# Optimization experiments

Hardware: AMD Instinct MI355X
Metric: run time of the kernel (lower is better)

Reference implementation:

```python
import jax, jax.numpy as jnp
import numpy as np

B, S, D, H = 2, 2048, 1024, 16
DK = D // H


def setup_inputs() -> dict:
    key = jax.random.key(0)
    ks = jax.random.split(key, 11)
    s = 1.0 / np.sqrt(D)
    inp = {
        "q": jax.random.normal(ks[0], (B, S, D), jnp.float32),
        "k": jax.random.normal(ks[1], (B, S, D), jnp.float32),
        "v": jax.random.normal(ks[2], (B, S, D), jnp.float32),
        "mask": jnp.tril(jnp.ones((S, S), jnp.int32))[None, None],  # causal [1,1,S,S]
        "w_q": jax.random.normal(ks[3], (D, D), jnp.float32) * s,
        "b_q": jax.random.normal(ks[4], (D,), jnp.float32) * 0.01,
        "w_k": jax.random.normal(ks[5], (D, D), jnp.float32) * s,
        "b_k": jax.random.normal(ks[6], (D,), jnp.float32) * 0.01,
        "w_v": jax.random.normal(ks[7], (D, D), jnp.float32) * s,
        "b_v": jax.random.normal(ks[8], (D,), jnp.float32) * 0.01,
        "w_o": jax.random.normal(ks[9], (D, D), jnp.float32) * s,
        "b_o": jax.random.normal(ks[10], (D,), jnp.float32) * 0.01,
    }
    return inp


def reference(q, k, v, mask, w_q, b_q, w_k, b_k, w_v, b_v, w_o, b_o):
    # Linear projections (torch Linear: x @ W.T + b)
    query = q @ w_q.T + b_q  # [B,S,D]
    key_ = k @ w_k.T + b_k
    value = v @ w_v.T + b_v
    # split heads -> [B,H,S,DK]
    def split(x):
        return x.reshape(B, S, H, DK).transpose(0, 2, 1, 3)
    qh, kh, vh = split(query), split(key_), split(value)
    scores = jnp.einsum("bhqd,bhkd->bhqk", qh, kh) / jnp.sqrt(jnp.float32(DK))
    scores = jnp.where(mask == 0, jnp.float32(-1e9), scores)
    attn = jax.nn.softmax(scores, axis=-1)
    out = jnp.einsum("bhqk,bhkd->bhqd", attn, vh)  # [B,H,S,DK]
    out = out.transpose(0, 2, 1, 3).reshape(B, S, D)
    return out @ w_o.T + b_o
```

## Files before the change

kernel.cpp:

```cpp
#include <hip/hip_runtime.h>


typedef __attribute__((ext_vector_type(8))) short bf16x8;
typedef __attribute__((ext_vector_type(4))) float floatx4;
typedef __attribute__((ext_vector_type(4))) unsigned short u16x4;

#define S_LEN 2048
#define D_MODEL 1024
#define N_HEADS 16
#define D_HEAD 64
#define M_ROWS 4096
#define QSCALE 0.18033688011112042f

__device__ __forceinline__ unsigned short f32_to_bf16(float f) {
  unsigned int u = __builtin_bit_cast(unsigned int, f);
  u += 0x7FFFu + ((u >> 16) & 1u);
  return (unsigned short)(u >> 16);
}

__device__ __forceinline__ void async_lds16(const unsigned short* g, unsigned short* l) {
  __builtin_amdgcn_global_load_lds(
      (const __attribute__((address_space(1))) unsigned int*)g,
      (__attribute__((address_space(3))) unsigned int*)l, 16, 0, 0);
}

__global__ __launch_bounds__(256) void cvt_w(
    const float* __restrict__ w0, const float* __restrict__ w1,
    const float* __restrict__ w2, const float* __restrict__ w3,
    unsigned short* __restrict__ dst) {
  const int z = blockIdx.y;
  const float* src = (z == 0) ? w0 : (z == 1) ? w1 : (z == 2) ? w2 : w3;
  unsigned short* d = dst + ((long)z << 20);
  const int n4 = 1 << 18;
  for (int i = blockIdx.x * 256 + threadIdx.x; i < n4; i += gridDim.x * 256) {
    float4 f = ((const float4*)src)[i];
    u16x4 o;
    o[0] = f32_to_bf16(f.x); o[1] = f32_to_bf16(f.y);
    o[2] = f32_to_bf16(f.z); o[3] = f32_to_bf16(f.w);
    ((u16x4*)d)[i] = o;
  }
}

__global__ __launch_bounds__(256) void cvt_x(
    const float* __restrict__ x0, const float* __restrict__ x1,
    const float* __restrict__ x2, unsigned short* __restrict__ dst) {
  const int z = blockIdx.y;
  const float* src = (z == 0) ? x0 : (z == 1) ? x1 : x2;
  unsigned short* d = dst + (long)z * M_ROWS * D_MODEL;
  const int n4 = (M_ROWS * D_MODEL) / 4;
  for (int i = blockIdx.x * 256 + threadIdx.x; i < n4; i += gridDim.x * 256) {
    float4 f = ((const float4*)src)[i];
    u16x4 o;
    o[0] = f32_to_bf16(f.x); o[1] = f32_to_bf16(f.y);
    o[2] = f32_to_bf16(f.z); o[3] = f32_to_bf16(f.w);
    ((u16x4*)d)[i] = o;
  }
}

#define GK 1024
#define GN 1024

template <bool XPRE>
__global__ __launch_bounds__(256, 3) void qkv_gemm(
    const float* __restrict__ Xq, const float* __restrict__ Xk, const float* __restrict__ Xv,
    const unsigned short* __restrict__ Xb,
    const unsigned short* __restrict__ Wb,
    const float* __restrict__ bq, const float* __restrict__ bk, const float* __restrict__ bv,
    unsigned short* __restrict__ Yq, unsigned short* __restrict__ Yk,
    unsigned short* __restrict__ Yvt) {
  __shared__ __align__(16) unsigned short As[128 * 64];
  __shared__ __align__(16) unsigned short Bs[128 * 64];

  const int z = blockIdx.z;
  const unsigned short* W = Wb + ((long)z << 20);
  const float* bias = (z == 0) ? bq : ((z == 1) ? bk : bv);

  const int r0 = blockIdx.x * 128;
  const int n0 = blockIdx.y * 128;
  const int tid = threadIdx.x;
  const int lane = tid & 63;
  const int wave = tid >> 6;
  const int quad = lane >> 4;
  const int ln = lane & 15;
  const int wm = (wave >> 1) * 64;
  const int wn = (wave & 1) * 64;

  floatx4 acc[4][4];
#pragma unroll
  for (int i = 0; i < 4; i++)
#pragma unroll
    for (int j = 0; j < 4; j++) acc[i][j] = (floatx4){0.f, 0.f, 0.f, 0.f};

  const int srow = (lane >> 3);
  const int scol8 = (lane & 7) * 8;
  const unsigned short* ApH = nullptr;
  const float* ApF = nullptr;
  if constexpr (XPRE) {
    ApH = Xb + (long)z * M_ROWS * D_MODEL;
  } else {
    ApF = (z == 0) ? Xq : ((z == 1) ? Xk : Xv);
  }

  for (int k0 = 0; k0 < GK; k0 += 64) {
    __syncthreads();
    if constexpr (XPRE) {
#pragma unroll
      for (int i = 0; i < 4; i++) {
        const int row = wave * 32 + i * 8;
        async_lds16(ApH + (long)(r0 + row + srow) * GK + k0 + scol8,
                    As + row * 64);
        async_lds16(W + (long)(n0 + row + srow) * GK + k0 + scol8,
                    Bs + row * 64);
      }
    } else {
      const int arow = tid >> 1;
      const int acol = (tid & 1) * 32;
      unsigned short ua[32] __attribute__((aligned(16)));
      float fa[32] __attribute__((aligned(16)));
#pragma unroll
      for (int c = 0; c < 8; c++)
        *(float4*)(fa + c * 4) = *(const float4*)(ApF + (long)(r0 + arow) * GK + k0 + acol + c * 4);
#pragma unroll
      for (int j = 0; j < 32; j++) ua[j] = f32_to_bf16(fa[j]);
      *(float4*)(As + arow * 64 + acol) = *(float4*)(ua);
      *(float4*)(As + arow * 64 + acol + 8) = *(float4*)(ua + 8);
      *(float4*)(As + arow * 64 + acol + 16) = *(float4*)(ua + 16);
      *(float4*)(As + arow * 64 + acol + 24) = *(float4*)(ua + 24);
#pragma unroll
      for (int i = 0; i < 4; i++) {
        const int row = wave * 32 + i * 8;
        async_lds16(W + (long)(n0 + row + srow) * GK + k0 + scol8,
                    Bs + row * 64);
      }
    }
    __syncthreads();

#pragma unroll
    for (int ks = 0; ks < 64; ks += 32) {
      bf16x8 af[4], bfr[4];
#pragma unroll
      for (int mt = 0; mt < 4; mt++)
        af[mt] = *(const bf16x8*)(As + (wm + mt * 16 + ln) * 64 + ks + quad * 8);
#pragma unroll
      for (int nt = 0; nt < 4; nt++)
        bfr[nt] = *(const bf16x8*)(Bs + (wn + nt * 16 + ln) * 64 + ks + quad * 8);
#pragma unroll
      for (int mt = 0; mt < 4; mt++)
#pragma unroll
        for (int nt = 0; nt < 4; nt++)
          acc[mt][nt] = __builtin_amdgcn_mfma_f32_16x16x32_bf16(af[mt], bfr[nt], acc[mt][nt], 0, 0, 0);
    }
  }

#pragma unroll
  for (int nt = 0; nt < 4; nt++) {
    const int n = n0 + wn + nt * 16 + ln;
    const float bv = bias[n];
#pragma unroll
    for (int mt = 0; mt < 4; mt++) {
      const int r = r0 + wm + mt * 16 + quad * 4;
      if (z == 2) {
        u16x4 pk;
#pragma unroll
        for (int reg = 0; reg < 4; reg++) pk[reg] = f32_to_bf16(acc[mt][nt][reg] + bv);
        *(u16x4*)(Yvt + (long)n * M_ROWS + r) = pk;
      } else if (z == 0) {
#pragma unroll
        for (int reg = 0; reg < 4; reg++)
          Yq[(long)(r + reg) * GN + n] = f32_to_bf16((acc[mt][nt][reg] + bv) * QSCALE);
      } else {
#pragma unroll
        for (int reg = 0; reg < 4; reg++)
          Yk[(long)(r + reg) * GN + n] = f32_to_bf16(acc[mt][nt][reg] + bv);
      }
    }
  }
}

__global__ __launch_bounds__(256, 3) void out_gemm(
    const unsigned short* __restrict__ X,
    const unsigned short* __restrict__ W,
    const float* __restrict__ bias,
    float* __restrict__ Y) {
  __shared__ __align__(16) unsigned short As[64 * 64];
  __shared__ __align__(16) unsigned short Bs[128 * 64];

  const int r0 = blockIdx.x * 64;
  const int n0 = blockIdx.y * 128;
  const int tid = threadIdx.x;
  const int lane = tid & 63;
  const int wave = tid >> 6;
  const int quad = lane >> 4;
  const int ln = lane & 15;
  const int wm = (wave >> 1) * 32;
  const int wn = (wave & 1) * 64;

  floatx4 acc[2][4];
#pragma unroll
  for (int i = 0; i < 2; i++)
#pragma unroll
    for (int j = 0; j < 4; j++) acc[i][j] = (floatx4){0.f, 0.f, 0.f, 0.f};

  const int srow = (lane >> 3);
  const int scol8 = (lane & 7) * 8;

  for (int k0 = 0; k0 < GK; k0 += 64) {
    __syncthreads();
#pragma unroll
    for (int i = 0; i < 2; i++) {
      const int row = wave * 16 + i * 8;
      async_lds16(X + (long)(r0 + row + srow) * GK + k0 + scol8, As + row * 64);
    }
#pragma unroll
    for (int i = 0; i < 4; i++) {
      const int row = wave * 32 + i * 8;
      async_lds16(W + (long)(n0 + row + srow) * GK + k0 + scol8, Bs + row * 64);
    }
    __syncthreads();

#pragma unroll
    for (int ks = 0; ks < 64; ks += 32) {
      bf16x8 af[2], bfr[4];
#pragma unroll
      for (int mt = 0; mt < 2; mt++)
        af[mt] = *(const bf16x8*)(As + (wm + mt * 16 + ln) * 64 + ks + quad * 8);
#pragma unroll
      for (int nt = 0; nt < 4; nt++)
        bfr[nt] = *(const bf16x8*)(Bs + (wn + nt * 16 + ln) * 64 + ks + quad * 8);
#pragma unroll
      for (int mt = 0; mt < 2; mt++)
#pragma unroll
        for (int nt = 0; nt < 4; nt++)
          acc[mt][nt] = __builtin_amdgcn_mfma_f32_16x16x32_bf16(af[mt], bfr[nt], acc[mt][nt], 0, 0, 0);
    }
  }

#pragma unroll
  for (int nt = 0; nt < 4; nt++) {
    const int n = n0 + wn + nt * 16 + ln;
    const float bv = bias[n];
#pragma unroll
    for (int mt = 0; mt < 2; mt++) {
      const int r = r0 + wm + mt * 16 + quad * 4;
#pragma unroll
      for (int reg = 0; reg < 4; reg++)
        Y[(long)(r + reg) * GN + n] = acc[mt][nt][reg] + bv;
    }
  }
}

#define PSTR 72

__global__ __launch_bounds__(64, 2) void attn_causal(
    const unsigned short* __restrict__ Q,
    const unsigned short* __restrict__ K,
    const unsigned short* __restrict__ Vt,
    unsigned short* __restrict__ O) {
  __shared__ __align__(16) unsigned short PbA[16 * PSTR];
  __shared__ __align__(16) unsigned short PbB[16 * PSTR];

  const int bh = blockIdx.x;
  const int pr = blockIdx.y;
  const int b = bh >> 4;
  const int h = bh & 15;

  const int lane = threadIdx.x;
  const int quad = lane >> 4;
  const int ln = lane & 15;

  const int s1 = pr, s2 = 127 - pr;
  const int q0A = s1 * 16, q0B = s2 * 16;
  const int nkt1 = (s1 >> 2) + 1;
  const int nkt2 = (s2 >> 2) + 1;

  const unsigned short* Qb = Q + (long)b * S_LEN * D_MODEL + h * D_HEAD;
  const unsigned short* Kb = K + (long)b * S_LEN * D_MODEL + h * D_HEAD;
  const unsigned short* Vb = Vt + (long)h * D_HEAD * M_ROWS + b * S_LEN;

  bf16x8 qfA[2], qfB[2];
  qfA[0] = *(const bf16x8*)(Qb + (long)(q0A + ln) * D_MODEL + quad * 8);
  qfA[1] = *(const bf16x8*)(Qb + (long)(q0A + ln) * D_MODEL + 32 + quad * 8);
  qfB[0] = *(const bf16x8*)(Qb + (long)(q0B + ln) * D_MODEL + quad * 8);
  qfB[1] = *(const bf16x8*)(Qb + (long)(q0B + ln) * D_MODEL + 32 + quad * 8);

  float mA = -1e30f, lA = 0.f, mB = -1e30f, lB = 0.f;
  floatx4 oA[4], oB[4];
#pragma unroll
  for (int nt = 0; nt < 4; nt++) {
    oA[nt] = (floatx4){0.f, 0.f, 0.f, 0.f};
    oB[nt] = (floatx4){0.f, 0.f, 0.f, 0.f};
  }

  auto loadKV = [&](bf16x8 (&kf)[4][2], bf16x8 (&vf)[4][2], int kt) {
    const int kv0 = kt * 64;
#pragma unroll
    for (int ct = 0; ct < 4; ct++) {
      const unsigned short* kp = Kb + (long)(kv0 + ct * 16 + ln) * D_MODEL + quad * 8;
      kf[ct][0] = *(const bf16x8*)(kp);
      kf[ct][1] = *(const bf16x8*)(kp + 32);
      const unsigned short* vp = Vb + (long)(ct * 16 + ln) * M_ROWS + kv0 + quad * 8;
      vf[ct][0] = *(const bf16x8*)(vp);
      vf[ct][1] = *(const bf16x8*)(vp + 32);
    }
  };

  auto iter = [&](bf16x8 (&kf)[4][2], bf16x8 (&vf)[4][2], int kt) {
    const int kv0 = kt * 64;
    const bool aAct = (kt < nkt1);

    floatx4 sB[4], sA[4];
#pragma unroll
    for (int ct = 0; ct < 4; ct++) {
      sB[ct] = (floatx4){0.f, 0.f, 0.f, 0.f};
      sB[ct] = __builtin_amdgcn_mfma_f32_16x16x32_bf16(kf[ct][0], qfB[0], sB[ct], 0, 0, 0);
      sB[ct] = __builtin_amdgcn_mfma_f32_16x16x32_bf16(kf[ct][1], qfB[1], sB[ct], 0, 0, 0);
    }
    if (aAct) {
#pragma unroll
      for (int ct = 0; ct < 4; ct++) {
        sA[ct] = (floatx4){0.f, 0.f, 0.f, 0.f};
        sA[ct] = __builtin_amdgcn_mfma_f32_16x16x32_bf16(kf[ct][0], qfA[0], sA[ct], 0, 0, 0);
        sA[ct] = __builtin_amdgcn_mfma_f32_16x16x32_bf16(kf[ct][1], qfA[1], sA[ct], 0, 0, 0);
      }
    }

    {
      float tmax = -1e30f;
      if (kt == nkt2 - 1) {
        const int qg = q0B + ln;
#pragma unroll
        for (int ct = 0; ct < 4; ct++) {
          const int kvb = kv0 + ct * 16 + quad * 4;
#pragma unroll
          for (int reg = 0; reg < 4; reg++) {
            float sv = sB[ct][reg];
            if (kvb + reg > qg) sv = -1e30f;
            sB[ct][reg] = sv;
            tmax = fmaxf(tmax, sv);
          }
        }
      } else {
#pragma unroll
        for (int ct = 0; ct < 4; ct++)
#pragma unroll
          for (int reg = 0; reg < 4; reg++) tmax = fmaxf(tmax, sB[ct][reg]);
      }
      tmax = fmaxf(tmax, __shfl_xor(tmax, 16, 64));
      tmax = fmaxf(tmax, __shfl_xor(tmax, 32, 64));
      const float mnew = fmaxf(mB, tmax);
      const float alpha = exp2f(mB - mnew);
      mB = mnew;
      float rsum = 0.f;
#pragma unroll
      for (int ct = 0; ct < 4; ct++) {
        u16x4 pk;
#pragma unroll
        for (int reg = 0; reg < 4; reg++) {
          const float p = exp2f(sB[ct][reg] - mB);
          rsum += p;
          pk[reg] = f32_to_bf16(p);
        }
        *(u16x4*)(PbB + ln * PSTR + ct * 16 + quad * 4) = pk;
      }
      rsum += __shfl_xor(rsum, 16, 64);
      rsum += __shfl_xor(rsum, 32, 64);
      lB = lB * alpha + rsum;
#pragma unroll
      for (int nt = 0; nt < 4; nt++)
#pragma unroll
        for (int reg = 0; reg < 4; reg++) oB[nt][reg] *= alpha;
    }

    if (aAct) {
      float tmax = -1e30f;
      if (kt == nkt1 - 1) {
        const int qg = q0A + ln;
#pragma unroll
        for (int ct = 0; ct < 4; ct++) {
          const int kvb = kv0 + ct * 16 + quad * 4;
#pragma unroll
          for (int reg = 0; reg < 4; reg++) {
            float sv = sA[ct][reg];
            if (kvb + reg > qg) sv = -1e30f;
            sA[ct][reg] = sv;
            tmax = fmaxf(tmax, sv);
          }
        }
      } else {
#pragma unroll
        for (int ct = 0; ct < 4; ct++)
#pragma unroll
          for (int reg = 0; reg < 4; reg++) tmax = fmaxf(tmax, sA[ct][reg]);
      }
      tmax = fmaxf(tmax, __shfl_xor(tmax, 16, 64));
      tmax = fmaxf(tmax, __shfl_xor(tmax, 32, 64));
      const float mnew = fmaxf(mA, tmax);
      const float alpha = exp2f(mA - mnew);
      mA = mnew;
      float rsum = 0.f;
#pragma unroll
      for (int ct = 0; ct < 4; ct++) {
        u16x4 pk;
#pragma unroll
        for (int reg = 0; reg < 4; reg++) {
          const float p = exp2f(sA[ct][reg] - mA);
          rsum += p;
          pk[reg] = f32_to_bf16(p);
        }
        *(u16x4*)(PbA + ln * PSTR + ct * 16 + quad * 4) = pk;
      }
      rsum += __shfl_xor(rsum, 16, 64);
      rsum += __shfl_xor(rsum, 32, 64);
      lA = lA * alpha + rsum;
#pragma unroll
      for (int nt = 0; nt < 4; nt++)
#pragma unroll
        for (int reg = 0; reg < 4; reg++) oA[nt][reg] *= alpha;
    }

    __builtin_amdgcn_wave_barrier();

    {
      bf16x8 p0 = *(const bf16x8*)(PbB + ln * PSTR + quad * 8);
      bf16x8 p1 = *(const bf16x8*)(PbB + ln * PSTR + 32 + quad * 8);
#pragma unroll
      for (int nt = 0; nt < 4; nt++) {
        oB[nt] = __builtin_amdgcn_mfma_f32_16x16x32_bf16(vf[nt][0], p0, oB[nt], 0, 0, 0);
        oB[nt] = __builtin_amdgcn_mfma_f32_16x16x32_bf16(vf[nt][1], p1, oB[nt], 0, 0, 0);
      }
    }
    if (aAct) {
      bf16x8 p0 = *(const bf16x8*)(PbA + ln * PSTR + quad * 8);
      bf16x8 p1 = *(const bf16x8*)(PbA + ln * PSTR + 32 + quad * 8);
#pragma unroll
      for (int nt = 0; nt < 4; nt++) {
        oA[nt] = __builtin_amdgcn_mfma_f32_16x16x32_bf16(vf[nt][0], p0, oA[nt], 0, 0, 0);
        oA[nt] = __builtin_amdgcn_mfma_f32_16x16x32_bf16(vf[nt][1], p1, oA[nt], 0, 0, 0);
      }
    }
    __builtin_amdgcn_wave_barrier();
  };

  bf16x8 kf0[4][2], vf0[4][2], kf1[4][2], vf1[4][2];
  loadKV(kf0, vf0, 0);
#pragma unroll 1
  for (int kt = 0; kt < nkt2; kt += 2) {
    if (kt + 1 < nkt2) loadKV(kf1, vf1, kt + 1);
    iter(kf0, vf0, kt);
    if (kt + 1 >= nkt2) break;
    if (kt + 2 < nkt2) loadKV(kf0, vf0, kt + 2);
    iter(kf1, vf1, kt + 1);
  }

  {
    const float inv = 1.0f / lA;
    unsigned short* op = O + (long)b * S_LEN * D_MODEL + (long)(q0A + ln) * D_MODEL + h * D_HEAD;
#pragma unroll
    for (int nt = 0; nt < 4; nt++) {
      u16x4 pk;
#pragma unroll
      for (int reg = 0; reg < 4; reg++) pk[reg] = f32_to_bf16(oA[nt][reg] * inv);
      *(u16x4*)(op + nt * 16 + quad * 4) = pk;
    }
  }
  {
    const float inv = 1.0f / lB;
    unsigned short* op = O + (long)b * S_LEN * D_MODEL + (long)(q0B + ln) * D_MODEL + h * D_HEAD;
#pragma unroll
    for (int nt = 0; nt < 4; nt++) {
      u16x4 pk;
#pragma unroll
      for (int reg = 0; reg < 4; reg++) pk[reg] = f32_to_bf16(oB[nt][reg] * inv);
      *(u16x4*)(op + nt * 16 + quad * 4) = pk;
    }
  }
}

extern "C" void kernel_launch(void* const* d_in, const int* in_sizes, int n_in,
                              void* d_out, int out_size, void* d_ws, size_t ws_size,
                              hipStream_t stream) {
  const float* q = (const float*)d_in[0];
  const float* k = (const float*)d_in[1];
  const float* v = (const float*)d_in[2];
  const float* w_q = (const float*)d_in[4];
  const float* b_q = (const float*)d_in[5];
  const float* w_k = (const float*)d_in[6];
  const float* b_k = (const float*)d_in[7];
  const float* w_v = (const float*)d_in[8];
  const float* b_v = (const float*)d_in[9];
  const float* w_o = (const float*)d_in[10];
  const float* b_o = (const float*)d_in[11];
  float* out = (float*)d_out;

  unsigned short* ws = (unsigned short*)d_ws;
  const long NE = (long)M_ROWS * D_MODEL;
  const bool xpre = (ws_size >= (size_t)7 * NE * sizeof(unsigned short));

  unsigned short *Qp, *Kp, *Vpt, *AO, *Wb, *Xb;
  if (xpre) {
    Qp = ws;
    Kp = ws + NE;
    Vpt = ws + 2 * NE;
    Wb = ws + 3 * NE;
    Xb = ws + 4 * NE;
    AO = ws + 4 * NE;
  } else {
    Qp = ws;
    Kp = ws + NE;
    Vpt = ws + 2 * NE;
    AO = ws + 3 * NE;
    Wb = ws + 4 * NE;
    Xb = nullptr;
  }

  cvt_w<<<dim3(256, 4), 256, 0, stream>>>(w_q, w_k, w_v, w_o, Wb);
  if (xpre) {
    cvt_x<<<dim3(512, 3), 256, 0, stream>>>(q, k, v, Xb);
    qkv_gemm<true><<<dim3(M_ROWS / 128, GN / 128, 3), 256, 0, stream>>>(
        q, k, v, Xb, Wb, b_q, b_k, b_v, Qp, Kp, Vpt);
  } else {
    qkv_gemm<false><<<dim3(M_ROWS / 128, GN / 128, 3), 256, 0, stream>>>(
        q, k, v, nullptr, Wb, b_q, b_k, b_v, Qp, Kp, Vpt);
  }
  attn_causal<<<dim3(2 * N_HEADS, 64), 64, 0, stream>>>(Qp, Kp, Vpt, AO);
  out_gemm<<<dim3(M_ROWS / 64, GN / 128), 256, 0, stream>>>(AO, Wb + 3 * (1 << 20), b_o, out);
}
```

Before: 282.2 us.

## Pad row strides of intermediate bf16 buffers to avoid channel/bank conflicts

Every bf16 intermediate (converted weights, converted inputs, Q, K, attention output) now uses a row stride of 1088 elements instead of 1024, and the transposed V uses 4160 instead of 4096. The aim is to break power-of-two strides that send many rows to the same memory channels or cache sets during the strided GEMM and attention loads. The convert kernels now launch one block per row to write the padded layout. The cost is a larger workspace, slightly less contiguous data, and a different xpre size threshold, which could disable the pre-conversion path if the workspace is too small.

```diff
diff --git a/kernel.cpp b/kernel.cpp
--- a/kernel.cpp
+++ b/kernel.cpp
@@ -12,6 +12,9 @@
 #define M_ROWS 4096
 #define QSCALE 0.18033688011112042f
 
+#define XSTR 1088
+#define VSTR 4160
+
 __device__ __forceinline__ unsigned short f32_to_bf16(float f) {
   unsigned int u = __builtin_bit_cast(unsigned int, f);
   u += 0x7FFFu + ((u >> 16) & 1u);
@@ -28,33 +31,31 @@
     const float* __restrict__ w0, const float* __restrict__ w1,
     const float* __restrict__ w2, const float* __restrict__ w3,
     unsigned short* __restrict__ dst) {
+  const int row = blockIdx.x;
   const int z = blockIdx.y;
-  const float* src = (z == 0) ? w0 : (z == 1) ? w1 : (z == 2) ? w2 : w3;
-  unsigned short* d = dst + ((long)z << 20);
-  const int n4 = 1 << 18;
-  for (int i = blockIdx.x * 256 + threadIdx.x; i < n4; i += gridDim.x * 256) {
-    float4 f = ((const float4*)src)[i];
-    u16x4 o;
-    o[0] = f32_to_bf16(f.x); o[1] = f32_to_bf16(f.y);
-    o[2] = f32_to_bf16(f.z); o[3] = f32_to_bf16(f.w);
-    ((u16x4*)d)[i] = o;
-  }
+  const float* src = ((z == 0) ? w0 : (z == 1) ? w1 : (z == 2) ? w2 : w3) + (long)row * 1024;
+  unsigned short* d = dst + (long)z * 1024 * XSTR + (long)row * XSTR;
+  const int tid = threadIdx.x;
+  float4 f = ((const float4*)src)[tid];
+  u16x4 o;
+  o[0] = f32_to_bf16(f.x); o[1] = f32_to_bf16(f.y);
+  o[2] = f32_to_bf16(f.z); o[3] = f32_to_bf16(f.w);
+  *(u16x4*)(d + tid * 4) = o;
 }
 
 __global__ __launch_bounds__(256) void cvt_x(
     const float* __restrict__ x0, const float* __restrict__ x1,
     const float* __restrict__ x2, unsigned short* __restrict__ dst) {
+  const int row = blockIdx.x;
   const int z = blockIdx.y;
-  const float* src = (z == 0) ? x0 : (z == 1) ? x1 : x2;
-  unsigned short* d = dst + (long)z * M_ROWS * D_MODEL;
-  const int n4 = (M_ROWS * D_MODEL) / 4;
-  for (int i = blockIdx.x * 256 + threadIdx.x; i < n4; i += gridDim.x * 256) {
-    float4 f = ((const float4*)src)[i];
-    u16x4 o;
-    o[0] = f32_to_bf16(f.x); o[1] = f32_to_bf16(f.y);
-    o[2] = f32_to_bf16(f.z); o[3] = f32_to_bf16(f.w);
-    ((u16x4*)d)[i] = o;
-  }
+  const float* src = ((z == 0) ? x0 : (z == 1) ? x1 : x2) + (long)row * 1024;
+  unsigned short* d = dst + (long)z * M_ROWS * XSTR + (long)row * XSTR;
+  const int tid = threadIdx.x;
+  float4 f = ((const float4*)src)[tid];
+  u16x4 o;
+  o[0] = f32_to_bf16(f.x); o[1] = f32_to_bf16(f.y);
+  o[2] = f32_to_bf16(f.z); o[3] = f32_to_bf16(f.w);
+  *(u16x4*)(d + tid * 4) = o;
 }
 
 #define GK 1024
@@ -72,7 +73,7 @@
   __shared__ __align__(16) unsigned short Bs[128 * 64];
 
   const int z = blockIdx.z;
-  const unsigned short* W = Wb + ((long)z << 20);
+  const unsigned short* W = Wb + (long)z * 1024 * XSTR;
   const float* bias = (z == 0) ? bq : ((z == 1) ? bk : bv);
 
   const int r0 = blockIdx.x * 128;
@@ -96,7 +97,7 @@
   const unsigned short* ApH = nullptr;
   const float* ApF = nullptr;
   if constexpr (XPRE) {
-    ApH = Xb + (long)z * M_ROWS * D_MODEL;
+    ApH = Xb + (long)z * M_ROWS * XSTR;
   } else {
     ApF = (z == 0) ? Xq : ((z == 1) ? Xk : Xv);
   }
@@ -107,9 +108,9 @@
 #pragma unroll
       for (int i = 0; i < 4; i++) {
         const int row = wave * 32 + i * 8;
-        async_lds16(ApH + (long)(r0 + row + srow) * GK + k0 + scol8,
+        async_lds16(ApH + (long)(r0 + row + srow) * XSTR + k0 + scol8,
                     As + row * 64);
-        async_lds16(W + (long)(n0 + row + srow) * GK + k0 + scol8,
+        async_lds16(W + (long)(n0 + row + srow) * XSTR + k0 + scol8,
                     Bs + row * 64);
       }
     } else {
@@ -129,7 +130,7 @@
 #pragma unroll
       for (int i = 0; i < 4; i++) {
         const int row = wave * 32 + i * 8;
-        async_lds16(W + (long)(n0 + row + srow) * GK + k0 + scol8,
+        async_lds16(W + (long)(n0 + row + srow) * XSTR + k0 + scol8,
                     Bs + row * 64);
       }
     }
@@ -163,15 +164,15 @@
         u16x4 pk;
 #pragma unroll
         for (int reg = 0; reg < 4; reg++) pk[reg] = f32_to_bf16(acc[mt][nt][reg] + bv);
-        *(u16x4*)(Yvt + (long)n * M_ROWS + r) = pk;
+        *(u16x4*)(Yvt + (long)n * VSTR + r) = pk;
       } else if (z == 0) {
 #pragma unroll
         for (int reg = 0; reg < 4; reg++)
-          Yq[(long)(r + reg) * GN + n] = f32_to_bf16((acc[mt][nt][reg] + bv) * QSCALE);
+          Yq[(long)(r + reg) * XSTR + n] = f32_to_bf16((acc[mt][nt][reg] + bv) * QSCALE);
       } else {
 #pragma unroll
         for (int reg = 0; reg < 4; reg++)
-          Yk[(long)(r + reg) * GN + n] = f32_to_bf16(acc[mt][nt][reg] + bv);
+          Yk[(long)(r + reg) * XSTR + n] = f32_to_bf16(acc[mt][nt][reg] + bv);
       }
     }
   }
@@ -209,12 +210,12 @@
 #pragma unroll
     for (int i = 0; i < 2; i++) {
       const int row = wave * 16 + i * 8;
-      async_lds16(X + (long)(r0 + row + srow) * GK + k0 + scol8, As + row * 64);
+      async_lds16(X + (long)(r0 + row + srow) * XSTR + k0 + scol8, As + row * 64);
     }
 #pragma unroll
     for (int i = 0; i < 4; i++) {
       const int row = wave * 32 + i * 8;
-      async_lds16(W + (long)(n0 + row + srow) * GK + k0 + scol8, Bs + row * 64);
+      async_lds16(W + (long)(n0 + row + srow) * XSTR + k0 + scol8, Bs + row * 64);
     }
     __syncthreads();
 
@@ -273,15 +274,15 @@
   const int nkt1 = (s1 >> 2) + 1;
   const int nkt2 = (s2 >> 2) + 1;
 
-  const unsigned short* Qb = Q + (long)b * S_LEN * D_MODEL + h * D_HEAD;
-  const unsigned short* Kb = K + (long)b * S_LEN * D_MODEL + h * D_HEAD;
-  const unsigned short* Vb = Vt + (long)h * D_HEAD * M_ROWS + b * S_LEN;
+  const unsigned short* Qb = Q + (long)b * S_LEN * XSTR + h * D_HEAD;
+  const unsigned short* Kb = K + (long)b * S_LEN * XSTR + h * D_HEAD;
+  const unsigned short* Vb = Vt + (long)h * D_HEAD * VSTR + b * S_LEN;
 
   bf16x8 qfA[2], qfB[2];
-  qfA[0] = *(const bf16x8*)(Qb + (long)(q0A + ln) * D_MODEL + quad * 8);
-  qfA[1] = *(const bf16x8*)(Qb + (long)(q0A + ln) * D_MODEL + 32 + quad * 8);
-  qfB[0] = *(const bf16x8*)(Qb + (long)(q0B + ln) * D_MODEL + quad * 8);
-  qfB[1] = *(const bf16x8*)(Qb + (long)(q0B + ln) * D_MODEL + 32 + quad * 8);
+  qfA[0] = *(const bf16x8*)(Qb + (long)(q0A + ln) * XSTR + quad * 8);
+  qfA[1] = *(const bf16x8*)(Qb + (long)(q0A + ln) * XSTR + 32 + quad * 8);
+  qfB[0] = *(const bf16x8*)(Qb + (long)(q0B + ln) * XSTR + quad * 8);
+  qfB[1] = *(const bf16x8*)(Qb + (long)(q0B + ln) * XSTR + 32 + quad * 8);
 
   float mA = -1e30f, lA = 0.f, mB = -1e30f, lB = 0.f;
   floatx4 oA[4], oB[4];
@@ -295,10 +296,10 @@
     const int kv0 = kt * 64;
 #pragma unroll
     for (int ct = 0; ct < 4; ct++) {
-      const unsigned short* kp = Kb + (long)(kv0 + ct * 16 + ln) * D_MODEL + quad * 8;
+      const unsigned short* kp = Kb + (long)(kv0 + ct * 16 + ln) * XSTR + quad * 8;
       kf[ct][0] = *(const bf16x8*)(kp);
       kf[ct][1] = *(const bf16x8*)(kp + 32);
-      const unsigned short* vp = Vb + (long)(ct * 16 + ln) * M_ROWS + kv0 + quad * 8;
+      const unsigned short* vp = Vb + (long)(ct * 16 + ln) * VSTR + kv0 + quad * 8;
       vf[ct][0] = *(const bf16x8*)(vp);
       vf[ct][1] = *(const bf16x8*)(vp + 32);
     }
@@ -454,7 +455,7 @@
 
   {
     const float inv = 1.0f / lA;
-    unsigned short* op = O + (long)b * S_LEN * D_MODEL + (long)(q0A + ln) * D_MODEL + h * D_HEAD;
+    unsigned short* op = O + (long)b * S_LEN * XSTR + (long)(q0A + ln) * XSTR + h * D_HEAD;
 #pragma unroll
     for (int nt = 0; nt < 4; nt++) {
       u16x4 pk;
@@ -465,7 +466,7 @@
   }
   {
     const float inv = 1.0f / lB;
-    unsigned short* op = O + (long)b * S_LEN * D_MODEL + (long)(q0B + ln) * D_MODEL + h * D_HEAD;
+    unsigned short* op = O + (long)b * S_LEN * XSTR + (long)(q0B + ln) * XSTR + h * D_HEAD;
 #pragma unroll
     for (int nt = 0; nt < 4; nt++) {
       u16x4 pk;
@@ -493,29 +494,33 @@
   float* out = (float*)d_out;
 
   unsigned short* ws = (unsigned short*)d_ws;
-  const long NE = (long)M_ROWS * D_MODEL;
-  const bool xpre = (ws_size >= (size_t)7 * NE * sizeof(unsigned short));
+  const long NR = (long)M_ROWS * XSTR;
+  const long NV = (long)1024 * VSTR;
+  const long NWALL = (long)4 * 1024 * XSTR;
+  const long NXALL = 3 * NR;
+  const long TOT_XPRE = 2 * NR + NV + NWALL + NXALL;
+  const bool xpre = (ws_size >= (size_t)TOT_XPRE * sizeof(unsigned short));
 
   unsigned short *Qp, *Kp, *Vpt, *AO, *Wb, *Xb;
   if (xpre) {
     Qp = ws;
-    Kp = ws + NE;
-    Vpt = ws + 2 * NE;
-    Wb = ws + 3 * NE;
-    Xb = ws + 4 * NE;
-    AO = ws + 4 * NE;
+    Kp = ws + NR;
+    Vpt = ws + 2 * NR;
+    Wb = ws + 2 * NR + NV;
+    Xb = Wb + NWALL;
+    AO = Xb;
   } else {
     Qp = ws;
-    Kp = ws + NE;
-    Vpt = ws + 2 * NE;
-    AO = ws + 3 * NE;
-    Wb = ws + 4 * NE;
+    Kp = ws + NR;
+    Vpt = ws + 2 * NR;
+    AO = ws + 2 * NR + NV;
+    Wb = AO + NR;
     Xb = nullptr;
   }
 
-  cvt_w<<<dim3(256, 4), 256, 0, stream>>>(w_q, w_k, w_v, w_o, Wb);
+  cvt_w<<<dim3(1024, 4), 256, 0, stream>>>(w_q, w_k, w_v, w_o, Wb);
   if (xpre) {
-    cvt_x<<<dim3(512, 3), 256, 0, stream>>>(q, k, v, Xb);
+    cvt_x<<<dim3(4096, 3), 256, 0, stream>>>(q, k, v, Xb);
     qkv_gemm<true><<<dim3(M_ROWS / 128, GN / 128, 3), 256, 0, stream>>>(
         q, k, v, Xb, Wb, b_q, b_k, b_v, Qp, Kp, Vpt);
   } else {
@@ -523,5 +528,5 @@
         q, k, v, nullptr, Wb, b_q, b_k, b_v, Qp, Kp, Vpt);
   }
   attn_causal<<<dim3(2 * N_HEADS, 64), 64, 0, stream>>>(Qp, Kp, Vpt, AO);
-  out_gemm<<<dim3(M_ROWS / 64, GN / 128), 256, 0, stream>>>(AO, Wb + 3 * (1 << 20), b_o, out);
-}
+  out_gemm<<<dim3(M_ROWS / 64, GN / 128), 256, 0, stream>>>(AO, Wb + 3 * (long)1024 * XSTR, b_o, out);
+}
```

Result: no change. 282.5 us (+0.1%).
